# Optimization experiments

Measured on AMD Instinct MI355X. Metric: run time of the kernel, lower is better.

The kernel has to match this reference:

```python
import jax, jax.numpy as jnp
import numpy as np

N, E, B = 50000, 800000, 16
IN_DIM, ED, HD, SD, NC = 64, 8, 128, 128, 8
T_STEPS = (8 + 16) // 2  # eval mode: (t_min + t_max) // 2 = 12


def setup_inputs() -> dict:
    key = jax.random.key(0)
    ks = jax.random.split(key, 12)
    s = 0.05  # small init scale so 12 residual steps stay bounded
    return {
        "x": jax.random.normal(ks[0], (N, IN_DIM), jnp.float32),
        "edge_index": jax.random.randint(ks[1], (2, E), 0, N, jnp.int64),
        "edge_attr": jax.random.normal(ks[2], (E, ED), jnp.float32),
        "batch": jnp.sort(jax.random.randint(ks[3], (N,), 0, B, jnp.int64)),
        "enc_w": jax.random.normal(ks[4], (IN_DIM, SD), jnp.float32) * s,
        "enc_b": jnp.zeros((SD,), jnp.float32),
        "msg_w": jax.random.normal(ks[5], (SD + ED, HD), jnp.float32) * s,
        "msg_b": jnp.zeros((HD,), jnp.float32),
        "up_w1": jax.random.normal(ks[6], (SD + HD, HD), jnp.float32) * s,
        "up_b1": jnp.zeros((HD,), jnp.float32),
        "up_w2": jax.random.normal(ks[7], (HD, SD), jnp.float32) * s,
        "up_b2": jnp.zeros((SD,), jnp.float32),
    }


def reference(x, edge_index, edge_attr, batch, enc_w, enc_b, msg_w, msg_b,
              up_w1, up_b1, up_w2, up_b2):
    src, dst = edge_index[0], edge_index[1]  # x_j = x[src], aggregate at dst
    # in-degree for mean aggregation (zero-degree nodes get 0, clamp avoids /0)
    deg = jax.ops.segment_sum(jnp.ones((E,), x.dtype), dst, num_segments=N)
    deg = jnp.clip(deg, 1.0)[:, None]

    # Encoder: Linear + ReLU
    state = jax.nn.relu(x @ enc_w + enc_b)  # [N, SD]

    for _ in range(T_STEPS):
        # message: relu(W_msg @ [h_j || e_ji])
        m = jax.nn.relu(jnp.concatenate([state[src], edge_attr], axis=-1) @ msg_w + msg_b)  # [E, HD]
        agg = jax.ops.segment_sum(m, dst, num_segments=N) / deg  # scatter-mean [N, HD]
        # update MLP on [h_i || m_bar_i]
        h = jax.nn.relu(jnp.concatenate([state, agg], axis=-1) @ up_w1 + up_b1)
        delta = h @ up_w2 + up_b2
        state = state + delta  # eval: no stochastic mask, no noise

    # Readout: per-graph mean over class channels
    class_ch = state[:, -NC:]  # [N, NC]
    cnt = jax.ops.segment_sum(jnp.ones((N,), x.dtype), batch, num_segments=B)
    logits = jax.ops.segment_sum(class_ch, batch, num_segments=B) / jnp.clip(cnt, 1.0)[:, None]
    return logits
```

## Files before the change

kernel.cpp:

```cpp
#include <hip/hip_runtime.h>
#include <hip/hip_bf16.h>

#define NN 50000
#define NE 800000
#define NB 16
#define T_STEPS 12
#define SCAN_B 196
#define EAW_BLOCKS 2048

typedef __attribute__((ext_vector_type(8))) short short8;
typedef __attribute__((ext_vector_type(4))) float f32x4;
typedef __attribute__((ext_vector_type(2))) float f32x2;
typedef unsigned short u16;
typedef unsigned int u32;

__device__ __forceinline__ float bf2f(u32 u) {
    union { u32 i; float f; } v; v.i = u << 16; return v.f;
}
__device__ __forceinline__ u16 f2bf(float f) {
    union { float f; u32 i; } v; v.f = f;
    u32 r = v.i + 0x7fffu + ((v.i >> 16) & 1u);
    return (u16)(r >> 16);
}
__device__ __forceinline__ f32x4 mfma16(short8 a, short8 b, f32x4 c) {
    return __builtin_amdgcn_mfma_f32_16x16x32_bf16(a, b, c, 0, 0, 0);
}

__device__ __forceinline__ u32 pk2_fp8(float o0, float o1) {
#if __has_builtin(__builtin_amdgcn_cvt_pk_fp8_f32)
    return (u32)__builtin_amdgcn_cvt_pk_fp8_f32(o0, o1, 0, false);
#else
    u32 a = 0;
    asm("v_cvt_pk_fp8_f32 %0, %1, %2" : "+v"(a) : "v"(o0), "v"(o1));
    return a;
#endif
}
__device__ __forceinline__ u32 pk4_fp8(float o0, float o1, float o2, float o3) {
    return (pk2_fp8(o0, o1) & 0xffffu) | (pk2_fp8(o2, o3) << 16);
}
__device__ __forceinline__ unsigned char f2fp8b(float v) {
    return (unsigned char)(pk2_fp8(v, 0.f) & 0xffu);
}

__device__ __forceinline__ void fp8x4f(u32 w, float& f0, float& f1, float& f2, float& f3) {
#if __has_builtin(__builtin_amdgcn_cvt_pk_f32_fp8)
    f32x2 r0 = __builtin_amdgcn_cvt_pk_f32_fp8((int)w, false);
    f32x2 r1 = __builtin_amdgcn_cvt_pk_f32_fp8((int)w, true);
    f0 = r0[0]; f1 = r0[1]; f2 = r1[0]; f3 = r1[1];
#else
    f32x2 r0, r1;
    u32 hi = w >> 16;
    asm("v_cvt_pk_f32_fp8 %0, %1" : "=v"(r0) : "v"(w));
    asm("v_cvt_pk_f32_fp8 %0, %1" : "=v"(r1) : "v"(hi));
    f0 = r0[0]; f1 = r0[1]; f2 = r1[0]; f3 = r1[1];
#endif
}

#define W1OFF 0
#define W2OFF 32768
#define WSOFF 49152
#define ENCOFF 65536
#define PACKN 73728


__global__ void k_hist(const int* __restrict__ dst, int* __restrict__ hist) {
    int e = blockIdx.x * 256 + threadIdx.x;
    if (e < NE) atomicAdd(&hist[dst[e]], 1);
}

__global__ void k_scanA(const int* __restrict__ hist, int* __restrict__ excl,
                        int* __restrict__ bsum) {
    __shared__ int sh[256];
    int t = threadIdx.x, b = blockIdx.x;
    int idx = b * 256 + t;
    int v = (idx < NN) ? hist[idx] : 0;
    sh[t] = v;
    __syncthreads();
    for (int off = 1; off < 256; off <<= 1) {
        int add = (t >= off) ? sh[t - off] : 0;
        __syncthreads();
        sh[t] += add;
        __syncthreads();
    }
    if (idx < NN) excl[idx] = sh[t] - v;
    if (t == 255) bsum[b] = sh[255];
}

__global__ void k_scanB(int* __restrict__ bsum) {
    __shared__ int sh[256];
    int t = threadIdx.x;
    int v = (t < SCAN_B) ? bsum[t] : 0;
    sh[t] = v;
    __syncthreads();
    for (int off = 1; off < 256; off <<= 1) {
        int add = (t >= off) ? sh[t - off] : 0;
        __syncthreads();
        sh[t] += add;
        __syncthreads();
    }
    if (t < SCAN_B) bsum[t] = sh[t] - v;
}

__global__ void k_scanC(const int* __restrict__ excl, const int* __restrict__ bsum,
                        int* __restrict__ rowptr, int* __restrict__ cursor) {
    int idx = blockIdx.x * 256 + threadIdx.x;
    if (idx < NN) {
        int r = excl[idx] + bsum[blockIdx.x];
        rowptr[idx] = r;
        cursor[idx] = r;
    }
    if (idx == 0) rowptr[NN] = NE;
}

__global__ void k_scatter(const int* __restrict__ src, const int* __restrict__ dst,
                          const float* __restrict__ eattr, int* __restrict__ cursor,
                          int* __restrict__ ssrc, u16* __restrict__ ea8) {
    int e = blockIdx.x * 256 + threadIdx.x;
    if (e >= NE) return;
    int d = dst[e];
    int pos = atomicAdd(&cursor[d], 1);
    ssrc[pos] = src[e];
    const float* ap = eattr + (size_t)e * 8;
    uint4 w;
    w.x = (u32)f2bf(ap[0]) | ((u32)f2bf(ap[1]) << 16);
    w.y = (u32)f2bf(ap[2]) | ((u32)f2bf(ap[3]) << 16);
    w.z = (u32)f2bf(ap[4]) | ((u32)f2bf(ap[5]) << 16);
    w.w = (u32)f2bf(ap[6]) | ((u32)f2bf(ap[7]) << 16);
    *(uint4*)(ea8 + (size_t)pos * 8) = w;
}

__global__ __launch_bounds__(256) void k_eaw(
    const u16* __restrict__ ea8, const float* __restrict__ msg_w,
    unsigned char* __restrict__ eaw) {
    const int tid = threadIdx.x;
    const int hex = tid & 15;
    const int esub = tid >> 4;
    float w[8][8];
#pragma unroll
    for (int k = 0; k < 8; ++k) {
        float4 v0 = *(const float4*)(msg_w + (size_t)(128 + k) * 128 + hex * 8);
        float4 v1 = *(const float4*)(msg_w + (size_t)(128 + k) * 128 + hex * 8 + 4);
        w[k][0] = v0.x; w[k][1] = v0.y; w[k][2] = v0.z; w[k][3] = v0.w;
        w[k][4] = v1.x; w[k][5] = v1.y; w[k][6] = v1.z; w[k][7] = v1.w;
    }
    int p = blockIdx.x * 16 + esub;
    if (p >= NE) return;
    uint4 ev = *(const uint4*)(ea8 + (size_t)p * 8);
    while (true) {
        int pn = p + EAW_BLOCKS * 16;
        bool more = pn < NE;
        uint4 evn;
        if (more) evn = *(const uint4*)(ea8 + (size_t)pn * 8);
        float ef[8];
        ef[0] = bf2f(ev.x & 0xffffu); ef[1] = bf2f(ev.x >> 16);
        ef[2] = bf2f(ev.y & 0xffffu); ef[3] = bf2f(ev.y >> 16);
        ef[4] = bf2f(ev.z & 0xffffu); ef[5] = bf2f(ev.z >> 16);
        ef[6] = bf2f(ev.w & 0xffffu); ef[7] = bf2f(ev.w >> 16);
        float o[8];
#pragma unroll
        for (int c = 0; c < 8; ++c) o[c] = ef[0] * w[0][c];
#pragma unroll
        for (int k = 1; k < 8; ++k)
#pragma unroll
            for (int c = 0; c < 8; ++c) o[c] += ef[k] * w[k][c];
        uint2 q;
        q.x = pk4_fp8(o[0], o[1], o[2], o[3]);
        q.y = pk4_fp8(o[4], o[5], o[6], o[7]);
        *(uint2*)(eaw + (size_t)p * 128 + hex * 8) = q;
        if (!more) break;
        p = pn;
        ev = evn;
    }
}

__global__ void k_pack(const float* __restrict__ up_w1, const float* __restrict__ up_w2,
                       const float* __restrict__ msg_w, const float* __restrict__ enc_w,
                       u16* __restrict__ packed) {
    int idx = blockIdx.x * 256 + threadIdx.x;
    if (idx >= PACKN) return;
    const float* srcp; int local;
    if (idx < W2OFF)        { srcp = up_w1; local = idx; }
    else if (idx < WSOFF)   { srcp = up_w2; local = idx - W2OFF; }
    else if (idx < ENCOFF)  { srcp = msg_w; local = idx - WSOFF; }
    else                    { srcp = enc_w; local = idx - ENCOFF; }
    int j = local & 7;
    int l = (local >> 3) & 63;
    int ntks = local >> 9;
    int nt = ntks & 7;
    int ks = ntks >> 3;
    int krow = ks * 32 + (l >> 4) * 8 + j;
    int col = nt * 16 + (l & 15);
    packed[idx] = f2bf(srcp[krow * 128 + col]);
}


__global__ __launch_bounds__(256) void k_encode(
    const float* __restrict__ x, const float* __restrict__ enc_b,
    const float* __restrict__ msg_b, const u16* __restrict__ packed,
    u16* __restrict__ state_h, unsigned char* __restrict__ swf8) {
    __shared__ u16 stage[4][2048];
    const int wv = threadIdx.x >> 6, l = threadIdx.x & 63;
    const int lr = l & 15, kb = l >> 4;
    const int rb = blockIdx.x * 64 + wv * 16;
    const int row = rb + lr;
    const int rowc = row < NN ? row : NN - 1;

    f32x4 acc[8] = {};
#pragma unroll
    for (int ks = 0; ks < 2; ++ks) {
        const float* ap = x + (size_t)rowc * 64 + ks * 32 + kb * 8;
        float4 a0 = *(const float4*)ap;
        float4 a1 = *(const float4*)(ap + 4);
        short8 a;
        a[0] = (short)f2bf(a0.x); a[1] = (short)f2bf(a0.y);
        a[2] = (short)f2bf(a0.z); a[3] = (short)f2bf(a0.w);
        a[4] = (short)f2bf(a1.x); a[5] = (short)f2bf(a1.y);
        a[6] = (short)f2bf(a1.z); a[7] = (short)f2bf(a1.w);
        const u16* bp = packed + ENCOFF + (size_t)(ks * 512 + l) * 8;
#pragma unroll
        for (int nt = 0; nt < 8; ++nt) {
            short8 b = *(const short8*)(bp + nt * 512);
            acc[nt] = mfma16(a, b, acc[nt]);
        }
    }
#pragma unroll
    for (int nt = 0; nt < 8; ++nt) {
        int col = nt * 16 + lr;
        float bias = enc_b[col];
#pragma unroll
        for (int j = 0; j < 4; ++j) {
            int rl = kb * 4 + j;
            int r = rb + rl;
            float v = acc[nt][j] + bias;
            v = v > 0.f ? v : 0.f;
            u16 h = f2bf(v);
            if (r < NN) state_h[(size_t)r * 128 + col] = h;
            int byte = (rl * 256 + col * 2) ^ ((rl & 7) << 4);
            *(u16*)((char*)stage[wv] + byte) = h;
        }
    }
    f32x4 acc3[8] = {};
#pragma unroll
    for (int ks = 0; ks < 4; ++ks) {
        int byte = (lr * 256 + ks * 64 + kb * 16) ^ ((lr & 7) << 4);
        short8 a = *(const short8*)((char*)stage[wv] + byte);
        const u16* bp = packed + WSOFF + (size_t)(ks * 512 + l) * 8;
#pragma unroll
        for (int nt = 0; nt < 8; ++nt) {
            short8 b = *(const short8*)(bp + nt * 512);
            acc3[nt] = mfma16(a, b, acc3[nt]);
        }
    }
#pragma unroll
    for (int nt = 0; nt < 8; ++nt) {
        int col = nt * 16 + lr;
        float bias = msg_b[col];
#pragma unroll
        for (int j = 0; j < 4; ++j) {
            int r = rb + kb * 4 + j;
            if (r < NN) swf8[(size_t)r * 128 + col] = f2fp8b(acc3[nt][j] + bias);
        }
    }
}


__global__ __launch_bounds__(256) void k_edge(
    const int* __restrict__ rowptr, const int* __restrict__ ssrc,
    const unsigned char* __restrict__ eaw, const unsigned char* __restrict__ swf8,
    u16* __restrict__ aggb) {
    const int wv = threadIdx.x >> 6, l = threadIdx.x & 63;
    const int slot = l >> 3;
    const int g = l & 7;
    const int n = blockIdx.x * 4 + wv;
    if (n >= NN) return;
    const int e0 = rowptr[n], e1 = rowptr[n + 1];
    float acc[16];
#pragma unroll
    for (int c = 0; c < 16; ++c) acc[c] = 0.f;

    int i = e0 + slot;
    uint4 qc = {0, 0, 0, 0}, sac = {0, 0, 0, 0};
    if (i < e1) {
        int sc = ssrc[i];
        qc = *(const uint4*)(eaw + (size_t)i * 128 + g * 16);
        sac = *(const uint4*)(swf8 + (size_t)sc * 128 + g * 16);
    }
    int inext = i + 8;
    int snext = (inext < e1) ? ssrc[inext] : 0;
    while (i < e1) {
        int i2 = inext + 8;
        int s2 = (i2 < e1) ? ssrc[i2] : 0;
        uint4 qn = {0, 0, 0, 0}, san = {0, 0, 0, 0};
        if (inext < e1) {
            qn = *(const uint4*)(eaw + (size_t)inext * 128 + g * 16);
            san = *(const uint4*)(swf8 + (size_t)snext * 128 + g * 16);
        }
        float ef[16], sw[16];
        fp8x4f(qc.x, ef[0], ef[1], ef[2], ef[3]);
        fp8x4f(qc.y, ef[4], ef[5], ef[6], ef[7]);
        fp8x4f(qc.z, ef[8], ef[9], ef[10], ef[11]);
        fp8x4f(qc.w, ef[12], ef[13], ef[14], ef[15]);
        fp8x4f(sac.x, sw[0], sw[1], sw[2], sw[3]);
        fp8x4f(sac.y, sw[4], sw[5], sw[6], sw[7]);
        fp8x4f(sac.z, sw[8], sw[9], sw[10], sw[11]);
        fp8x4f(sac.w, sw[12], sw[13], sw[14], sw[15]);
#pragma unroll
        for (int c = 0; c < 16; ++c) {
            float m = sw[c] + ef[c];
            acc[c] += m > 0.f ? m : 0.f;
        }
        qc = qn; sac = san;
        i = inext;
        inext = i2;
        snext = s2;
    }
#pragma unroll
    for (int c = 0; c < 16; ++c) acc[c] += __shfl_xor(acc[c], 8);
#pragma unroll
    for (int c = 0; c < 16; ++c) acc[c] += __shfl_xor(acc[c], 16);
#pragma unroll
    for (int c = 0; c < 16; ++c) acc[c] += __shfl_xor(acc[c], 32);
    if (slot == 0) {
        int dg = e1 - e0;
        float inv = 1.f / (float)(dg > 0 ? dg : 1);
        uint4 w0, w1;
        w0.x = (u32)f2bf(acc[0] * inv)  | ((u32)f2bf(acc[1] * inv) << 16);
        w0.y = (u32)f2bf(acc[2] * inv)  | ((u32)f2bf(acc[3] * inv) << 16);
        w0.z = (u32)f2bf(acc[4] * inv)  | ((u32)f2bf(acc[5] * inv) << 16);
        w0.w = (u32)f2bf(acc[6] * inv)  | ((u32)f2bf(acc[7] * inv) << 16);
        w1.x = (u32)f2bf(acc[8] * inv)  | ((u32)f2bf(acc[9] * inv) << 16);
        w1.y = (u32)f2bf(acc[10] * inv) | ((u32)f2bf(acc[11] * inv) << 16);
        w1.z = (u32)f2bf(acc[12] * inv) | ((u32)f2bf(acc[13] * inv) << 16);
        w1.w = (u32)f2bf(acc[14] * inv) | ((u32)f2bf(acc[15] * inv) << 16);
        *(uint4*)(aggb + (size_t)n * 128 + g * 16) = w0;
        *(uint4*)(aggb + (size_t)n * 128 + g * 16 + 8) = w1;
    }
}


__global__ __launch_bounds__(128) void k_update(
    const float* __restrict__ up_b1, const float* __restrict__ up_b2,
    const float* __restrict__ msg_b, const u16* __restrict__ packed,
    const u16* __restrict__ aggb, u16* __restrict__ state_h,
    unsigned char* __restrict__ swf8) {
    __shared__ u16 stage[2][2][2048];
    const int wv = threadIdx.x >> 6, l = threadIdx.x & 63;
    const int lr = l & 15, kb = l >> 4;
    const int rbase = blockIdx.x * 64 + wv * 32;

    f32x4 acc[2][8] = {};
#pragma unroll
    for (int ks = 0; ks < 8; ++ks) {
        short8 a[2];
#pragma unroll
        for (int rt = 0; rt < 2; ++rt) {
            int row = rbase + rt * 16 + lr;
            int rowc = row < NN ? row : NN - 1;
            const u16* abase = (ks < 4)
                ? (state_h + (size_t)rowc * 128 + ks * 32 + kb * 8)
                : (aggb + (size_t)rowc * 128 + (ks - 4) * 32 + kb * 8);
            a[rt] = *(const short8*)abase;
        }
        const u16* bp = packed + W1OFF + (size_t)(ks * 512 + l) * 8;
#pragma unroll
        for (int nt = 0; nt < 8; ++nt) {
            short8 b = *(const short8*)(bp + nt * 512);
            acc[0][nt] = mfma16(a[0], b, acc[0][nt]);
            acc[1][nt] = mfma16(a[1], b, acc[1][nt]);
        }
    }
#pragma unroll
    for (int nt = 0; nt < 8; ++nt) {
        int col = nt * 16 + lr;
        float b1v = up_b1[col];
#pragma unroll
        for (int rt = 0; rt < 2; ++rt) {
#pragma unroll
            for (int j = 0; j < 4; ++j) {
                int rl = kb * 4 + j;
                float v = acc[rt][nt][j] + b1v;
                v = v > 0.f ? v : 0.f;
                int byte = (rl * 256 + col * 2) ^ ((rl & 7) << 4);
                *(u16*)((char*)stage[wv][rt] + byte) = f2bf(v);
            }
        }
    }
    f32x4 acc2[2][8] = {};
#pragma unroll
    for (int ks = 0; ks < 4; ++ks) {
        int byte = (lr * 256 + ks * 64 + kb * 16) ^ ((lr & 7) << 4);
        short8 a[2];
        a[0] = *(const short8*)((char*)stage[wv][0] + byte);
        a[1] = *(const short8*)((char*)stage[wv][1] + byte);
        const u16* bp = packed + W2OFF + (size_t)(ks * 512 + l) * 8;
#pragma unroll
        for (int nt = 0; nt < 8; ++nt) {
            short8 b = *(const short8*)(bp + nt * 512);
            acc2[0][nt] = mfma16(a[0], b, acc2[0][nt]);
            acc2[1][nt] = mfma16(a[1], b, acc2[1][nt]);
        }
    }
#pragma unroll
    for (int rt = 0; rt < 2; ++rt) {
#pragma unroll
        for (int nt = 0; nt < 8; ++nt) {
            int col = nt * 16 + lr;
            float b2v = up_b2[col];
#pragma unroll
            for (int j = 0; j < 4; ++j) {
                int rl = kb * 4 + j;
                int r = rbase + rt * 16 + rl;
                int rc = r < NN ? r : NN - 1;
                float sold = bf2f((u32)state_h[(size_t)rc * 128 + col]);
                float snew = sold + acc2[rt][nt][j] + b2v;
                u16 hb = f2bf(snew);
                if (r < NN) state_h[(size_t)r * 128 + col] = hb;
                int byte = (rl * 256 + col * 2) ^ ((rl & 7) << 4);
                *(u16*)((char*)stage[wv][rt] + byte) = hb;
            }
        }
    }
    f32x4 acc3[2][8] = {};
#pragma unroll
    for (int ks = 0; ks < 4; ++ks) {
        int byte = (lr * 256 + ks * 64 + kb * 16) ^ ((lr & 7) << 4);
        short8 a[2];
        a[0] = *(const short8*)((char*)stage[wv][0] + byte);
        a[1] = *(const short8*)((char*)stage[wv][1] + byte);
        const u16* bp = packed + WSOFF + (size_t)(ks * 512 + l) * 8;
#pragma unroll
        for (int nt = 0; nt < 8; ++nt) {
            short8 b = *(const short8*)(bp + nt * 512);
            acc3[0][nt] = mfma16(a[0], b, acc3[0][nt]);
            acc3[1][nt] = mfma16(a[1], b, acc3[1][nt]);
        }
    }
#pragma unroll
    for (int rt = 0; rt < 2; ++rt) {
#pragma unroll
        for (int nt = 0; nt < 8; ++nt) {
            int col = nt * 16 + lr;
            float bias = msg_b[col];
#pragma unroll
            for (int j = 0; j < 4; ++j) {
                int r = rbase + rt * 16 + kb * 4 + j;
                if (r < NN) swf8[(size_t)r * 128 + col] = f2fp8b(acc3[rt][nt][j] + bias);
            }
        }
    }
}


__global__ void k_logits(const u16* __restrict__ state_h, const int* __restrict__ batch,
                         float* __restrict__ out) {
    __shared__ float red[256];
    int b = blockIdx.x, t = threadIdx.x;
    int ch = t & 7, sub = t >> 3;
    int lo = 0, hi = NN;
    while (lo < hi) { int m = (lo + hi) >> 1; if (batch[m] < b) lo = m + 1; else hi = m; }
    int s0 = lo;
    lo = 0; hi = NN;
    while (lo < hi) { int m = (lo + hi) >> 1; if (batch[m] < b + 1) lo = m + 1; else hi = m; }
    int s1 = lo;
    float acc = 0.f;
    for (int n = s0 + sub; n < s1; n += 32)
        acc += bf2f((u32)state_h[(size_t)n * 128 + 120 + ch]);
    red[t] = acc;
    __syncthreads();
    for (int off = 16; off >= 1; off >>= 1) {
        if (sub < off) red[t] += red[t + off * 8];
        __syncthreads();
    }
    if (sub == 0) {
        int c = s1 - s0;
        float cnt = (float)(c > 0 ? c : 1);
        out[b * 8 + ch] = red[ch] / cnt;
    }
}


extern "C" void kernel_launch(void* const* d_in, const int* in_sizes, int n_in,
                              void* d_out, int out_size, void* d_ws, size_t ws_size,
                              hipStream_t stream) {
    (void)in_sizes; (void)n_in;
    const float* x      = (const float*)d_in[0];
    const int*   eidx   = (const int*)d_in[1];
    const float* eattr  = (const float*)d_in[2];
    const int*   batch  = (const int*)d_in[3];
    const float* enc_w  = (const float*)d_in[4];
    const float* enc_b  = (const float*)d_in[5];
    const float* msg_w  = (const float*)d_in[6];
    const float* msg_b  = (const float*)d_in[7];
    const float* up_w1  = (const float*)d_in[8];
    const float* up_b1  = (const float*)d_in[9];
    const float* up_w2  = (const float*)d_in[10];
    const float* up_b2  = (const float*)d_in[11];
    const int* esrc = eidx;
    const int* edst = eidx + NE;

    char* p = (char*)d_ws;
    size_t off = 0;
    auto carve = [&](size_t bytes) -> char* {
        char* r = p + off;
        off += (bytes + 255) & ~(size_t)255;
        return r;
    };
    u16* state_h   = (u16*)carve((size_t)NN * 128 * 2);
    u16* aggb      = (u16*)carve((size_t)NN * 128 * 2);
    unsigned char* swf8 = (unsigned char*)carve((size_t)NN * 128);
    int* ssrc      = (int*)carve((size_t)NE * 4);
    u16* ea8       = (u16*)carve((size_t)NE * 8 * 2);
    unsigned char* eaw = (unsigned char*)carve((size_t)NE * 128);
    int* rowptr    = (int*)carve((size_t)(NN + 1) * 4);
    int* cursor    = (int*)carve((size_t)NN * 4);
    int* hist      = (int*)carve((size_t)NN * 4);
    int* sexcl     = (int*)carve((size_t)NN * 4);
    int* bsum      = (int*)carve((size_t)256 * 4);
    u16* packed    = (u16*)carve((size_t)PACKN * 2);
    if (off > ws_size) {
        hipMemsetAsync(d_out, 0xFF, (size_t)out_size * 4, stream);
        return;
    }

    hipMemsetAsync(hist, 0, (size_t)NN * 4, stream);
    k_hist<<<(NE + 255) / 256, 256, 0, stream>>>(edst, hist);
    k_scanA<<<SCAN_B, 256, 0, stream>>>(hist, sexcl, bsum);
    k_scanB<<<1, 256, 0, stream>>>(bsum);
    k_scanC<<<SCAN_B, 256, 0, stream>>>(sexcl, bsum, rowptr, cursor);
    k_scatter<<<(NE + 255) / 256, 256, 0, stream>>>(esrc, edst, eattr, cursor, ssrc, ea8);
    k_eaw<<<EAW_BLOCKS, 256, 0, stream>>>(ea8, msg_w, eaw);
    k_pack<<<(PACKN + 255) / 256, 256, 0, stream>>>(up_w1, up_w2, msg_w, enc_w, packed);
    k_encode<<<(NN + 63) / 64, 256, 0, stream>>>(x, enc_b, msg_b, packed, state_h, swf8);
    for (int t = 0; t < T_STEPS; ++t) {
        k_edge<<<(NN + 3) / 4, 256, 0, stream>>>(rowptr, ssrc, eaw, swf8, aggb);
        k_update<<<(NN + 63) / 64, 128, 0, stream>>>(up_b1, up_b2, msg_b, packed, aggb,
                                                     state_h, swf8);
    }
    k_logits<<<NB, 256, 0, stream>>>(state_h, batch, (float*)d_out);
}
```

Measured before the change: 1.037 ms.

## Recompute edge-attribute projection inside edge kernel instead of materializing per-edge fp8 tensor

Drops the k_eaw pre-pass and its E×128 fp8 buffer, which every message-passing step re-read in full. Instead, each edge kernel loads the 8 bf16 edge attributes per edge and does the 8×8 matvec against msg_w held in registers. This trades a large per-step memory stream for extra FMAs and a heavier register footprint. Each lane now covers 8 channels, so a wave handles 4 edges per iteration instead of 8, and the projection keeps full fp32 precision rather than fp8.

```diff
diff --git a/kernel.cpp b/kernel.cpp
--- a/kernel.cpp
+++ b/kernel.cpp
@@ -6,7 +6,6 @@
 #define NB 16
 #define T_STEPS 12
 #define SCAN_B 196
-#define EAW_BLOCKS 2048
 
 typedef __attribute__((ext_vector_type(8))) short short8;
 typedef __attribute__((ext_vector_type(4))) float f32x4;
@@ -34,9 +33,6 @@
     asm("v_cvt_pk_fp8_f32 %0, %1, %2" : "+v"(a) : "v"(o0), "v"(o1));
     return a;
 #endif
-}
-__device__ __forceinline__ u32 pk4_fp8(float o0, float o1, float o2, float o3) {
-    return (pk2_fp8(o0, o1) & 0xffffu) | (pk2_fp8(o2, o3) << 16);
 }
 __device__ __forceinline__ unsigned char f2fp8b(float v) {
     return (unsigned char)(pk2_fp8(v, 0.f) & 0xffu);
@@ -127,50 +123,6 @@
     w.z = (u32)f2bf(ap[4]) | ((u32)f2bf(ap[5]) << 16);
     w.w = (u32)f2bf(ap[6]) | ((u32)f2bf(ap[7]) << 16);
     *(uint4*)(ea8 + (size_t)pos * 8) = w;
-}
-
-__global__ __launch_bounds__(256) void k_eaw(
-    const u16* __restrict__ ea8, const float* __restrict__ msg_w,
-    unsigned char* __restrict__ eaw) {
-    const int tid = threadIdx.x;
-    const int hex = tid & 15;
-    const int esub = tid >> 4;
-    float w[8][8];
-#pragma unroll
-    for (int k = 0; k < 8; ++k) {
-        float4 v0 = *(const float4*)(msg_w + (size_t)(128 + k) * 128 + hex * 8);
-        float4 v1 = *(const float4*)(msg_w + (size_t)(128 + k) * 128 + hex * 8 + 4);
-        w[k][0] = v0.x; w[k][1] = v0.y; w[k][2] = v0.z; w[k][3] = v0.w;
-        w[k][4] = v1.x; w[k][5] = v1.y; w[k][6] = v1.z; w[k][7] = v1.w;
-    }
-    int p = blockIdx.x * 16 + esub;
-    if (p >= NE) return;
-    uint4 ev = *(const uint4*)(ea8 + (size_t)p * 8);
-    while (true) {
-        int pn = p + EAW_BLOCKS * 16;
-        bool more = pn < NE;
-        uint4 evn;
-        if (more) evn = *(const uint4*)(ea8 + (size_t)pn * 8);
-        float ef[8];
-        ef[0] = bf2f(ev.x & 0xffffu); ef[1] = bf2f(ev.x >> 16);
-        ef[2] = bf2f(ev.y & 0xffffu); ef[3] = bf2f(ev.y >> 16);
-        ef[4] = bf2f(ev.z & 0xffffu); ef[5] = bf2f(ev.z >> 16);
-        ef[6] = bf2f(ev.w & 0xffffu); ef[7] = bf2f(ev.w >> 16);
-        float o[8];
-#pragma unroll
-        for (int c = 0; c < 8; ++c) o[c] = ef[0] * w[0][c];
-#pragma unroll
-        for (int k = 1; k < 8; ++k)
-#pragma unroll
-            for (int c = 0; c < 8; ++c) o[c] += ef[k] * w[k][c];
-        uint2 q;
-        q.x = pk4_fp8(o[0], o[1], o[2], o[3]);
-        q.y = pk4_fp8(o[4], o[5], o[6], o[7]);
-        *(uint2*)(eaw + (size_t)p * 128 + hex * 8) = q;
-        if (!more) break;
-        p = pn;
-        ev = evn;
-    }
 }
 
 __global__ void k_pack(const float* __restrict__ up_w1, const float* __restrict__ up_w2,
@@ -266,74 +218,83 @@
 
 __global__ __launch_bounds__(256) void k_edge(
     const int* __restrict__ rowptr, const int* __restrict__ ssrc,
-    const unsigned char* __restrict__ eaw, const unsigned char* __restrict__ swf8,
-    u16* __restrict__ aggb) {
+    const u16* __restrict__ ea8, const unsigned char* __restrict__ swf8,
+    const float* __restrict__ msg_w, u16* __restrict__ aggb) {
     const int wv = threadIdx.x >> 6, l = threadIdx.x & 63;
-    const int slot = l >> 3;
-    const int g = l & 7;
+    const int slot = l >> 4;
+    const int cl = l & 15;
+    float w[8][8];
+#pragma unroll
+    for (int k = 0; k < 8; ++k) {
+        float4 v0 = *(const float4*)(msg_w + (size_t)(128 + k) * 128 + cl * 8);
+        float4 v1 = *(const float4*)(msg_w + (size_t)(128 + k) * 128 + cl * 8 + 4);
+        w[k][0] = v0.x; w[k][1] = v0.y; w[k][2] = v0.z; w[k][3] = v0.w;
+        w[k][4] = v1.x; w[k][5] = v1.y; w[k][6] = v1.z; w[k][7] = v1.w;
+    }
     const int n = blockIdx.x * 4 + wv;
     if (n >= NN) return;
     const int e0 = rowptr[n], e1 = rowptr[n + 1];
-    float acc[16];
-#pragma unroll
-    for (int c = 0; c < 16; ++c) acc[c] = 0.f;
+    float acc[8];
+#pragma unroll
+    for (int c = 0; c < 8; ++c) acc[c] = 0.f;
 
     int i = e0 + slot;
-    uint4 qc = {0, 0, 0, 0}, sac = {0, 0, 0, 0};
+    uint4 ec = {0, 0, 0, 0};
+    uint2 sc = {0, 0};
     if (i < e1) {
-        int sc = ssrc[i];
-        qc = *(const uint4*)(eaw + (size_t)i * 128 + g * 16);
-        sac = *(const uint4*)(swf8 + (size_t)sc * 128 + g * 16);
-    }
-    int inext = i + 8;
+        int s = ssrc[i];
+        ec = *(const uint4*)(ea8 + (size_t)i * 8);
+        sc = *(const uint2*)(swf8 + (size_t)s * 128 + cl * 8);
+    }
+    int inext = i + 4;
     int snext = (inext < e1) ? ssrc[inext] : 0;
     while (i < e1) {
-        int i2 = inext + 8;
+        int i2 = inext + 4;
         int s2 = (i2 < e1) ? ssrc[i2] : 0;
-        uint4 qn = {0, 0, 0, 0}, san = {0, 0, 0, 0};
+        uint4 en = {0, 0, 0, 0};
+        uint2 sn = {0, 0};
         if (inext < e1) {
-            qn = *(const uint4*)(eaw + (size_t)inext * 128 + g * 16);
-            san = *(const uint4*)(swf8 + (size_t)snext * 128 + g * 16);
-        }
-        float ef[16], sw[16];
-        fp8x4f(qc.x, ef[0], ef[1], ef[2], ef[3]);
-        fp8x4f(qc.y, ef[4], ef[5], ef[6], ef[7]);
-        fp8x4f(qc.z, ef[8], ef[9], ef[10], ef[11]);
-        fp8x4f(qc.w, ef[12], ef[13], ef[14], ef[15]);
-        fp8x4f(sac.x, sw[0], sw[1], sw[2], sw[3]);
-        fp8x4f(sac.y, sw[4], sw[5], sw[6], sw[7]);
-        fp8x4f(sac.z, sw[8], sw[9], sw[10], sw[11]);
-        fp8x4f(sac.w, sw[12], sw[13], sw[14], sw[15]);
-#pragma unroll
-        for (int c = 0; c < 16; ++c) {
-            float m = sw[c] + ef[c];
+            en = *(const uint4*)(ea8 + (size_t)inext * 8);
+            sn = *(const uint2*)(swf8 + (size_t)snext * 128 + cl * 8);
+        }
+        float ef[8];
+        ef[0] = bf2f(ec.x & 0xffffu); ef[1] = bf2f(ec.x >> 16);
+        ef[2] = bf2f(ec.y & 0xffffu); ef[3] = bf2f(ec.y >> 16);
+        ef[4] = bf2f(ec.z & 0xffffu); ef[5] = bf2f(ec.z >> 16);
+        ef[6] = bf2f(ec.w & 0xffffu); ef[7] = bf2f(ec.w >> 16);
+        float o[8];
+#pragma unroll
+        for (int c = 0; c < 8; ++c) o[c] = ef[0] * w[0][c];
+#pragma unroll
+        for (int k = 1; k < 8; ++k)
+#pragma unroll
+            for (int c = 0; c < 8; ++c) o[c] += ef[k] * w[k][c];
+        float sw[8];
+        fp8x4f(sc.x, sw[0], sw[1], sw[2], sw[3]);
+        fp8x4f(sc.y, sw[4], sw[5], sw[6], sw[7]);
+#pragma unroll
+        for (int c = 0; c < 8; ++c) {
+            float m = sw[c] + o[c];
             acc[c] += m > 0.f ? m : 0.f;
         }
-        qc = qn; sac = san;
+        ec = en; sc = sn;
         i = inext;
         inext = i2;
         snext = s2;
     }
 #pragma unroll
-    for (int c = 0; c < 16; ++c) acc[c] += __shfl_xor(acc[c], 8);
-#pragma unroll
-    for (int c = 0; c < 16; ++c) acc[c] += __shfl_xor(acc[c], 16);
-#pragma unroll
-    for (int c = 0; c < 16; ++c) acc[c] += __shfl_xor(acc[c], 32);
+    for (int c = 0; c < 8; ++c) acc[c] += __shfl_xor(acc[c], 16);
+#pragma unroll
+    for (int c = 0; c < 8; ++c) acc[c] += __shfl_xor(acc[c], 32);
     if (slot == 0) {
         int dg = e1 - e0;
         float inv = 1.f / (float)(dg > 0 ? dg : 1);
-        uint4 w0, w1;
-        w0.x = (u32)f2bf(acc[0] * inv)  | ((u32)f2bf(acc[1] * inv) << 16);
-        w0.y = (u32)f2bf(acc[2] * inv)  | ((u32)f2bf(acc[3] * inv) << 16);
-        w0.z = (u32)f2bf(acc[4] * inv)  | ((u32)f2bf(acc[5] * inv) << 16);
-        w0.w = (u32)f2bf(acc[6] * inv)  | ((u32)f2bf(acc[7] * inv) << 16);
-        w1.x = (u32)f2bf(acc[8] * inv)  | ((u32)f2bf(acc[9] * inv) << 16);
-        w1.y = (u32)f2bf(acc[10] * inv) | ((u32)f2bf(acc[11] * inv) << 16);
-        w1.z = (u32)f2bf(acc[12] * inv) | ((u32)f2bf(acc[13] * inv) << 16);
-        w1.w = (u32)f2bf(acc[14] * inv) | ((u32)f2bf(acc[15] * inv) << 16);
-        *(uint4*)(aggb + (size_t)n * 128 + g * 16) = w0;
-        *(uint4*)(aggb + (size_t)n * 128 + g * 16 + 8) = w1;
+        uint4 w0;
+        w0.x = (u32)f2bf(acc[0] * inv) | ((u32)f2bf(acc[1] * inv) << 16);
+        w0.y = (u32)f2bf(acc[2] * inv) | ((u32)f2bf(acc[3] * inv) << 16);
+        w0.z = (u32)f2bf(acc[4] * inv) | ((u32)f2bf(acc[5] * inv) << 16);
+        w0.w = (u32)f2bf(acc[6] * inv) | ((u32)f2bf(acc[7] * inv) << 16);
+        *(uint4*)(aggb + (size_t)n * 128 + cl * 8) = w0;
     }
 }
 
@@ -510,7 +471,6 @@
     unsigned char* swf8 = (unsigned char*)carve((size_t)NN * 128);
     int* ssrc      = (int*)carve((size_t)NE * 4);
     u16* ea8       = (u16*)carve((size_t)NE * 8 * 2);
-    unsigned char* eaw = (unsigned char*)carve((size_t)NE * 128);
     int* rowptr    = (int*)carve((size_t)(NN + 1) * 4);
     int* cursor    = (int*)carve((size_t)NN * 4);
     int* hist      = (int*)carve((size_t)NN * 4);
@@ -528,11 +488,10 @@
     k_scanB<<<1, 256, 0, stream>>>(bsum);
     k_scanC<<<SCAN_B, 256, 0, stream>>>(sexcl, bsum, rowptr, cursor);
     k_scatter<<<(NE + 255) / 256, 256, 0, stream>>>(esrc, edst, eattr, cursor, ssrc, ea8);
-    k_eaw<<<EAW_BLOCKS, 256, 0, stream>>>(ea8, msg_w, eaw);
     k_pack<<<(PACKN + 255) / 256, 256, 0, stream>>>(up_w1, up_w2, msg_w, enc_w, packed);
     k_encode<<<(NN + 63) / 64, 256, 0, stream>>>(x, enc_b, msg_b, packed, state_h, swf8);
     for (int t = 0; t < T_STEPS; ++t) {
-        k_edge<<<(NN + 3) / 4, 256, 0, stream>>>(rowptr, ssrc, eaw, swf8, aggb);
+        k_edge<<<(NN + 3) / 4, 256, 0, stream>>>(rowptr, ssrc, ea8, swf8, msg_w, aggb);
         k_update<<<(NN + 63) / 64, 128, 0, stream>>>(up_b1, up_b2, msg_b, packed, aggb,
                                                      state_h, swf8);
     }
```

Measured after the change: 1.681 ms. +62.0%, slower.

## Split update rows across four waves and use bf16 dot2 for edge-attr projection

Applied to the files above, without the earlier changes.

k_update now uses 256 threads per block, with each wave handling 16 rows instead of 32. This halves the per-thread accumulator registers and raises occupancy, but each block now loads the B weight fragments twice as often. Separately, k_eaw packs the edge-attribute weights into bf16 pairs and uses the fdot2 bf16 intrinsic when the compiler provides it. That reduces VALU work and register use but rounds the weights to bf16.

```diff
diff --git a/kernel.cpp b/kernel.cpp
--- a/kernel.cpp
+++ b/kernel.cpp
@@ -13,6 +13,16 @@
 typedef __attribute__((ext_vector_type(2))) float f32x2;
 typedef unsigned short u16;
 typedef unsigned int u32;
+
+#if __has_builtin(__builtin_amdgcn_fdot2_f32_bf16)
+#define HAS_DOT2_BF16 1
+typedef __attribute__((ext_vector_type(2))) __bf16 bf16x2;
+__device__ __forceinline__ bf16x2 as_bf16x2(u32 v) {
+    union { u32 i; bf16x2 h; } u; u.i = v; return u.h;
+}
+#else
+#define HAS_DOT2_BF16 0
+#endif
 
 __device__ __forceinline__ float bf2f(u32 u) {
     union { u32 i; float f; } v; v.i = u << 16; return v.f;
@@ -135,6 +145,18 @@
     const int tid = threadIdx.x;
     const int hex = tid & 15;
     const int esub = tid >> 4;
+#if HAS_DOT2_BF16
+    u32 wp[4][8];
+#pragma unroll
+    for (int kk = 0; kk < 4; ++kk) {
+#pragma unroll
+        for (int c = 0; c < 8; ++c) {
+            float w0 = msg_w[(size_t)(128 + 2 * kk) * 128 + hex * 8 + c];
+            float w1 = msg_w[(size_t)(128 + 2 * kk + 1) * 128 + hex * 8 + c];
+            wp[kk][c] = (u32)f2bf(w0) | ((u32)f2bf(w1) << 16);
+        }
+    }
+#else
     float w[8][8];
 #pragma unroll
     for (int k = 0; k < 8; ++k) {
@@ -143,6 +165,7 @@
         w[k][0] = v0.x; w[k][1] = v0.y; w[k][2] = v0.z; w[k][3] = v0.w;
         w[k][4] = v1.x; w[k][5] = v1.y; w[k][6] = v1.z; w[k][7] = v1.w;
     }
+#endif
     int p = blockIdx.x * 16 + esub;
     if (p >= NE) return;
     uint4 ev = *(const uint4*)(ea8 + (size_t)p * 8);
@@ -151,18 +174,31 @@
         bool more = pn < NE;
         uint4 evn;
         if (more) evn = *(const uint4*)(ea8 + (size_t)pn * 8);
+        float o[8];
+#if HAS_DOT2_BF16
+        u32 ep[4] = {ev.x, ev.y, ev.z, ev.w};
+#pragma unroll
+        for (int c = 0; c < 8; ++c) o[c] = 0.f;
+#pragma unroll
+        for (int kk = 0; kk < 4; ++kk) {
+            bf16x2 ea2 = as_bf16x2(ep[kk]);
+#pragma unroll
+            for (int c = 0; c < 8; ++c)
+                o[c] = __builtin_amdgcn_fdot2_f32_bf16(ea2, as_bf16x2(wp[kk][c]), o[c], false);
+        }
+#else
         float ef[8];
         ef[0] = bf2f(ev.x & 0xffffu); ef[1] = bf2f(ev.x >> 16);
         ef[2] = bf2f(ev.y & 0xffffu); ef[3] = bf2f(ev.y >> 16);
         ef[4] = bf2f(ev.z & 0xffffu); ef[5] = bf2f(ev.z >> 16);
         ef[6] = bf2f(ev.w & 0xffffu); ef[7] = bf2f(ev.w >> 16);
-        float o[8];
 #pragma unroll
         for (int c = 0; c < 8; ++c) o[c] = ef[0] * w[0][c];
 #pragma unroll
         for (int k = 1; k < 8; ++k)
 #pragma unroll
             for (int c = 0; c < 8; ++c) o[c] += ef[k] * w[k][c];
+#endif
         uint2 q;
         q.x = pk4_fp8(o[0], o[1], o[2], o[3]);
         q.y = pk4_fp8(o[4], o[5], o[6], o[7]);
@@ -338,35 +374,30 @@
 }
 
 
-__global__ __launch_bounds__(128) void k_update(
+__global__ __launch_bounds__(256) void k_update(
     const float* __restrict__ up_b1, const float* __restrict__ up_b2,
     const float* __restrict__ msg_b, const u16* __restrict__ packed,
     const u16* __restrict__ aggb, u16* __restrict__ state_h,
     unsigned char* __restrict__ swf8) {
-    __shared__ u16 stage[2][2][2048];
+    __shared__ u16 stage[4][2048];
     const int wv = threadIdx.x >> 6, l = threadIdx.x & 63;
     const int lr = l & 15, kb = l >> 4;
-    const int rbase = blockIdx.x * 64 + wv * 32;
-
-    f32x4 acc[2][8] = {};
+    const int rbase = blockIdx.x * 64 + wv * 16;
+    const int row = rbase + lr;
+    const int rowc = row < NN ? row : NN - 1;
+
+    f32x4 acc[8] = {};
 #pragma unroll
     for (int ks = 0; ks < 8; ++ks) {
-        short8 a[2];
-#pragma unroll
-        for (int rt = 0; rt < 2; ++rt) {
-            int row = rbase + rt * 16 + lr;
-            int rowc = row < NN ? row : NN - 1;
-            const u16* abase = (ks < 4)
-                ? (state_h + (size_t)rowc * 128 + ks * 32 + kb * 8)
-                : (aggb + (size_t)rowc * 128 + (ks - 4) * 32 + kb * 8);
-            a[rt] = *(const short8*)abase;
-        }
+        const u16* abase = (ks < 4)
+            ? (state_h + (size_t)rowc * 128 + ks * 32 + kb * 8)
+            : (aggb + (size_t)rowc * 128 + (ks - 4) * 32 + kb * 8);
+        short8 a = *(const short8*)abase;
         const u16* bp = packed + W1OFF + (size_t)(ks * 512 + l) * 8;
 #pragma unroll
         for (int nt = 0; nt < 8; ++nt) {
             short8 b = *(const short8*)(bp + nt * 512);
-            acc[0][nt] = mfma16(a[0], b, acc[0][nt]);
-            acc[1][nt] = mfma16(a[1], b, acc[1][nt]);
+            acc[nt] = mfma16(a, b, acc[nt]);
         }
     }
 #pragma unroll
@@ -374,78 +405,63 @@
         int col = nt * 16 + lr;
         float b1v = up_b1[col];
 #pragma unroll
-        for (int rt = 0; rt < 2; ++rt) {
-#pragma unroll
-            for (int j = 0; j < 4; ++j) {
-                int rl = kb * 4 + j;
-                float v = acc[rt][nt][j] + b1v;
-                v = v > 0.f ? v : 0.f;
-                int byte = (rl * 256 + col * 2) ^ ((rl & 7) << 4);
-                *(u16*)((char*)stage[wv][rt] + byte) = f2bf(v);
-            }
-        }
-    }
-    f32x4 acc2[2][8] = {};
+        for (int j = 0; j < 4; ++j) {
+            int rl = kb * 4 + j;
+            float v = acc[nt][j] + b1v;
+            v = v > 0.f ? v : 0.f;
+            int byte = (rl * 256 + col * 2) ^ ((rl & 7) << 4);
+            *(u16*)((char*)stage[wv] + byte) = f2bf(v);
+        }
+    }
+    f32x4 acc2[8] = {};
 #pragma unroll
     for (int ks = 0; ks < 4; ++ks) {
         int byte = (lr * 256 + ks * 64 + kb * 16) ^ ((lr & 7) << 4);
-        short8 a[2];
-        a[0] = *(const short8*)((char*)stage[wv][0] + byte);
-        a[1] = *(const short8*)((char*)stage[wv][1] + byte);
+        short8 a = *(const short8*)((char*)stage[wv] + byte);
         const u16* bp = packed + W2OFF + (size_t)(ks * 512 + l) * 8;
 #pragma unroll
         for (int nt = 0; nt < 8; ++nt) {
             short8 b = *(const short8*)(bp + nt * 512);
-            acc2[0][nt] = mfma16(a[0], b, acc2[0][nt]);
-            acc2[1][nt] = mfma16(a[1], b, acc2[1][nt]);
-        }
-    }
-#pragma unroll
-    for (int rt = 0; rt < 2; ++rt) {
-#pragma unroll
-        for (int nt = 0; nt < 8; ++nt) {
-            int col = nt * 16 + lr;
-            float b2v = up_b2[col];
-#pragma unroll
-            for (int j = 0; j < 4; ++j) {
-                int rl = kb * 4 + j;
-                int r = rbase + rt * 16 + rl;
-                int rc = r < NN ? r : NN - 1;
-                float sold = bf2f((u32)state_h[(size_t)rc * 128 + col]);
-                float snew = sold + acc2[rt][nt][j] + b2v;
-                u16 hb = f2bf(snew);
-                if (r < NN) state_h[(size_t)r * 128 + col] = hb;
-                int byte = (rl * 256 + col * 2) ^ ((rl & 7) << 4);
-                *(u16*)((char*)stage[wv][rt] + byte) = hb;
-            }
-        }
-    }
-    f32x4 acc3[2][8] = {};
+            acc2[nt] = mfma16(a, b, acc2[nt]);
+        }
+    }
+#pragma unroll
+    for (int nt = 0; nt < 8; ++nt) {
+        int col = nt * 16 + lr;
+        float b2v = up_b2[col];
+#pragma unroll
+        for (int j = 0; j < 4; ++j) {
+            int rl = kb * 4 + j;
+            int r = rbase + rl;
+            int rc = r < NN ? r : NN - 1;
+            float sold = bf2f((u32)state_h[(size_t)rc * 128 + col]);
+            float snew = sold + acc2[nt][j] + b2v;
+            u16 hb = f2bf(snew);
+            if (r < NN) state_h[(size_t)r * 128 + col] = hb;
+            int byte = (rl * 256 + col * 2) ^ ((rl & 7) << 4);
+            *(u16*)((char*)stage[wv] + byte) = hb;
+        }
+    }
+    f32x4 acc3[8] = {};
 #pragma unroll
     for (int ks = 0; ks < 4; ++ks) {
         int byte = (lr * 256 + ks * 64 + kb * 16) ^ ((lr & 7) << 4);
-        short8 a[2];
-        a[0] = *(const short8*)((char*)stage[wv][0] + byte);
-        a[1] = *(const short8*)((char*)stage[wv][1] + byte);
+        short8 a = *(const short8*)((char*)stage[wv] + byte);
         const u16* bp = packed + WSOFF + (size_t)(ks * 512 + l) * 8;
 #pragma unroll
         for (int nt = 0; nt < 8; ++nt) {
             short8 b = *(const short8*)(bp + nt * 512);
-            acc3[0][nt] = mfma16(a[0], b, acc3[0][nt]);
-            acc3[1][nt] = mfma16(a[1], b, acc3[1][nt]);
-        }
-    }
-#pragma unroll
-    for (int rt = 0; rt < 2; ++rt) {
-#pragma unroll
-        for (int nt = 0; nt < 8; ++nt) {
-            int col = nt * 16 + lr;
-            float bias = msg_b[col];
-#pragma unroll
-            for (int j = 0; j < 4; ++j) {
-                int r = rbase + rt * 16 + kb * 4 + j;
-                if (r < NN) swf8[(size_t)r * 128 + col] = f2fp8b(acc3[rt][nt][j] + bias);
-            }
+            acc3[nt] = mfma16(a, b, acc3[nt]);
+        }
+    }
+#pragma unroll
+    for (int nt = 0; nt < 8; ++nt) {
+        int col = nt * 16 + lr;
+        float bias = msg_b[col];
+#pragma unroll
+        for (int j = 0; j < 4; ++j) {
+            int r = rbase + kb * 4 + j;
+            if (r < NN) swf8[(size_t)r * 128 + col] = f2fp8b(acc3[nt][j] + bias);
         }
     }
 }
@@ -533,7 +549,7 @@
     k_encode<<<(NN + 63) / 64, 256, 0, stream>>>(x, enc_b, msg_b, packed, state_h, swf8);
     for (int t = 0; t < T_STEPS; ++t) {
         k_edge<<<(NN + 3) / 4, 256, 0, stream>>>(rowptr, ssrc, eaw, swf8, aggb);
-        k_update<<<(NN + 63) / 64, 128, 0, stream>>>(up_b1, up_b2, msg_b, packed, aggb,
+        k_update<<<(NN + 63) / 64, 256, 0, stream>>>(up_b1, up_b2, msg_b, packed, aggb,
                                                      state_h, swf8);
     }
     k_logits<<<NB, 256, 0, stream>>>(state_h, batch, (float*)d_out);
```

Result: slower. 1.077 ms (+3.8%).
